# Kernel optimization log

Hardware: AMD Instinct MI355X
Metric: run time of the kernel (lower is better)

Reference implementation:

```python
import jax, jax.numpy as jnp
import numpy as np
import math

H = 512        # hidden_dim
DEPTH = 5
KS = 3         # kernel size
DELTA = 0.1
M = 104        # timestamp == seq_len
NC = 5
B = 512
BN_EPS = 1e-5


def setup_inputs() -> dict:
    key = jax.random.key(0)
    ks = jax.random.split(key, 16)
    inp = {}
    inp['x'] = jax.random.normal(ks[0], (B, 1, M), dtype=jnp.float32)
    # CausalCNN: depth conv layers (first is 1->H, rest H->H), each followed by BN
    inp['conv_w0'] = jax.random.normal(ks[1], (H, 1, KS), dtype=jnp.float32) * (1.0 / np.sqrt(KS))
    inp['conv_b0'] = jnp.zeros((H,), jnp.float32)
    inp['conv_w'] = jax.random.normal(ks[2], (DEPTH - 1, H, H, KS), dtype=jnp.float32) * (1.0 / np.sqrt(H * KS))
    inp['conv_b'] = jnp.zeros((DEPTH - 1, H), jnp.float32)
    inp['bn_gamma'] = jnp.ones((DEPTH, H), jnp.float32)
    inp['bn_beta'] = jnp.zeros((DEPTH, H), jnp.float32)
    # input_proj
    inp['proj_w'] = jax.random.normal(ks[3], (H, H), dtype=jnp.float32) * (1.0 / np.sqrt(H))
    inp['proj_b'] = jnp.zeros((H,), jnp.float32)
    # ZOH layers: A = -0.01*I + 0.001*randn, B = 0.01*randn [H,1], C = 0.01*randn [1,H]
    eye = jnp.eye(H, dtype=jnp.float32)
    inp['A_all'] = -0.01 * eye[None] + 0.001 * jax.random.normal(ks[4], (DEPTH, H, H), dtype=jnp.float32)
    inp['B_all'] = 0.01 * jax.random.normal(ks[5], (DEPTH, H, 1), dtype=jnp.float32)
    inp['C_all'] = 0.01 * jax.random.normal(ks[6], (DEPTH, 1, H), dtype=jnp.float32)
    # fc_temp: Linear(H,H) -> BN1d(H) -> GELU -> Dropout(eval) -> Linear(H,NC)
    inp['fc1_w'] = jax.random.normal(ks[7], (H, H), dtype=jnp.float32) * (1.0 / np.sqrt(H))
    inp['fc1_b'] = jnp.zeros((H,), jnp.float32)
    inp['fc_bn_gamma'] = jnp.ones((H,), jnp.float32)
    inp['fc_bn_beta'] = jnp.zeros((H,), jnp.float32)
    inp['fc2_w'] = jax.random.normal(ks[8], (NC, H), dtype=jnp.float32) * (1.0 / np.sqrt(H))
    inp['fc2_b'] = jnp.zeros((NC,), jnp.float32)
    return inp


def _causal_conv(x, w, b):
    # x: [B, Cin, T], w: [Cout, Cin, K] -> left-pad K-1 (equivalent to pad both + trim right)
    y = jax.lax.conv_general_dilated(x, w, window_strides=(1,), padding=[(KS - 1, 0)],
                                     dimension_numbers=('NCH', 'OIH', 'NCH'))
    return y + b[None, :, None]


def _bn_ct(x, g, b):
    # BatchNorm1d over [B, C, T], batch statistics (training-mode normalization)
    m = x.mean(axis=(0, 2), keepdims=True)
    v = x.var(axis=(0, 2), keepdims=True)
    return g[None, :, None] * (x - m) * jax.lax.rsqrt(v + BN_EPS) + b[None, :, None]


def _pos_encoding(T, d):
    pos = jnp.arange(T, dtype=jnp.float32)[:, None]
    div = jnp.exp(jnp.arange(0, d, 2, dtype=jnp.float32) * (-math.log(10000.0) / d))
    pe = jnp.zeros((T, d), jnp.float32)
    pe = pe.at[:, 0::2].set(jnp.sin(pos * div))
    pe = pe.at[:, 1::2].set(jnp.cos(pos * div))
    return pe


def _zoh_kbar(A, Bv, Cv):
    # A: [H,H], Bv: [H,1], Cv: [1,H] -> normalized K_bar [M]
    A_bar = jax.scipy.linalg.expm(DELTA * A)
    I = jnp.eye(H, dtype=A.dtype)
    A_inv = jnp.linalg.inv(A + 0.001 * I)
    B_bar = A_inv @ (A_bar - I) @ (DELTA * Bv)  # [H,1]
    # term_k = C @ A_bar^k @ B_bar; sequential vector recurrence replaces matrix powers
    def step(v, _):
        term = (Cv @ v)[0, 0]
        return A_bar @ v, term
    _, terms = jax.lax.scan(step, B_bar, None, length=M)  # [M]
    Kb = jnp.flip(terms, axis=0)
    return Kb / (jnp.linalg.norm(Kb) + 1e-6)


def reference(x, conv_w0, conv_b0, conv_w, conv_b, bn_gamma, bn_beta, proj_w, proj_b,
              A_all, B_all, C_all, fc1_w, fc1_b, fc_bn_gamma, fc_bn_beta, fc2_w, fc2_b):
    # CausalCNN
    h = jax.nn.relu(_bn_ct(_causal_conv(x, conv_w0, conv_b0), bn_gamma[0], bn_beta[0]))
    for i in range(DEPTH - 1):
        h = jax.nn.relu(_bn_ct(_causal_conv(h, conv_w[i], conv_b[i]), bn_gamma[i + 1], bn_beta[i + 1]))
    h = jnp.transpose(h, (0, 2, 1))  # [B, T, H]
    # positional encoding + input projection
    h = h + _pos_encoding(M, H)[None]
    h = jnp.einsum('bth,oh->bto', h, proj_w) + proj_b
    # stacked ZOH kernels: each layer multiplies x by its normalized K_bar along time
    Ks = jax.vmap(_zoh_kbar)(A_all, B_all, C_all)  # [DEPTH, M]
    h = h * jnp.prod(Ks, axis=0)[None, :, None]
    # mean pool over time, then fc_temp (BN with batch stats, dropout = identity/eval)
    h = h.mean(axis=1)  # [B, H]
    h = jnp.dot(h, fc1_w.T) + fc1_b
    m = h.mean(axis=0, keepdims=True)
    v = h.var(axis=0, keepdims=True)
    h = fc_bn_gamma * (h - m) * jax.lax.rsqrt(v + BN_EPS) + fc_bn_beta
    h = jax.nn.gelu(h, approximate=False)
    logits = jnp.dot(h, fc2_w.T) + fc2_b  # [B, NC]
    return logits
```

## Files before the change

kernel.cpp:

```cpp
#include <hip/hip_runtime.h>
#include <cstdio>
#include <cmath>
#include <cstdint>

constexpr int BM = 512 * 104;
constexpr float BN_EPS = 1e-5f;

constexpr size_t SZ_BF   = (size_t)BM * 512 * 2;
constexpr size_t SZ_MAT5 = (size_t)5 * 512 * 512 * 4;
constexpr size_t OFF_YB0 = 0;
constexpr size_t OFF_YB1 = OFF_YB0 + SZ_BF;
constexpr size_t OFF_WT2 = OFF_YB1 + SZ_BF;
constexpr size_t OFF_X   = OFF_WT2 + 6291456;
constexpr size_t OFF_T1  = OFF_X   + SZ_MAT5;
constexpr size_t OFF_T2  = OFF_T1  + SZ_MAT5;
constexpr size_t OFF_E   = OFF_T2  + SZ_MAT5;
constexpr size_t OFF_MW  = OFF_E   + SZ_MAT5;
constexpr size_t OFF_P2  = OFF_MW  + SZ_MAT5;
constexpr size_t OFF_P4  = OFF_P2  + SZ_MAT5;
constexpr size_t OFF_ROWT= OFF_P4  + SZ_MAT5;
constexpr size_t OFF_COLS= OFF_ROWT + 655360;
constexpr size_t OFF_COLS2=OFF_COLS + 655360;
constexpr size_t OFF_PIVI= OFF_COLS2 + 655360;
constexpr size_t OFF_PJT = OFF_PIVI + 81920;
// ... 197 lines not shown
        } else if (mode == 5) {
            for (int j = 0; j < 4; ++j) v[j] += aux[col0 + j] * sc2;
        } else if (mode == 7) {
            float pv[4];
            for (int j = 0; j < 4; ++j) {
                int col = col0 + j;
                pv[j] = ((row == col) ? 0.5f : 0.0f) + aux[(long)row * 512 + col] * (1.0f / 6.0f)
                        + v[j] * (1.0f / 24.0f);
            }
            *(float4*)&Cp[base] = make_float4(pv[0], pv[1], pv[2], pv[3]);
        } else if (mode == 8) {
            for (int j = 0; j < 4; ++j) {
                v[j] += aux[col0 + j];
                cs1[j] += v[j]; cs2[j] += v[j] * v[j];
            }
        }
        *(float4*)&C[base] = make_float4(v[0], v[1], v[2], v[3]);
    }
    if (mode == 8) {
        __syncthreads();
        float* s1s = sm;
        float* s2s = sm + 1024;
#pragma unroll
        for (int j = 0; j < 4; ++j) {
            s1s[ty * 64 + tx * 4 + j] = cs1[j];
            s2s[ty * 64 + tx * 4 + j] = cs2[j];
        }
        __syncthreads();
        if (tid < 64) {
            double a = 0.0, b = 0.0;
#pragma unroll
            for (int t = 0; t < 16; ++t) { a += s1s[t * 64 + tid]; b += s2s[t * 64 + tid]; }
            atomicAdd(&st1[n0 + tid], a);
            atomicAdd(&st2[n0 + tid], b);
        }
    }
}

__global__ __launch_bounds__(256) void k_elim3(
    const float* __restrict__ MWin, float* __restrict__ MWout,
    const float* __restrict__ PIVI, float* __restrict__ PIVN,
    const float* __restrict__ COLSc, float* __restrict__ COLSn, int pc, int pcn)
{
    __shared__ float As[64 * 68];
    __shared__ float Rs[64 * 68];
    __shared__ float fv[64];
    __shared__ int perm[64];
    __shared__ int arr[64];
    __shared__ int pividx;
    __shared__ float dv;
    int z = blockIdx.z;
    MWin += (long)z * 262144; MWout += (long)z * 262144;
    PIVI += z * 4096; COLSc += (long)z * 32768; COLSn += (long)z * 32768;
    int m0 = blockIdx.x * 64, n0 = blockIdx.y * 64;
    int tid = threadIdx.x;
    int tx = tid & 15, ty = tid >> 4;

    if (n0 == pc) {
        for (int it = 0; it < 16; ++it) {
            int idx = it * 256 + tid;
            int r = idx >> 6, c = idx & 63;
            Rs[r * 68 + c] = PIVI[r * 64 + c];
        }
        __syncthreads();
    } else {
        {
            int m = tid >> 2, kb = (tid & 3) * 16;
#pragma unroll
            for (int u = 0; u < 4; ++u) {
                float4 v = *(const float4*)&PIVI[m * 64 + kb + u * 4];
                As[(kb + u * 4 + 0) * 68 + m] = v.x;
                As[(kb + u * 4 + 1) * 68 + m] = v.y;
                As[(kb + u * 4 + 2) * 68 + m] = v.z;
                As[(kb + u * 4 + 3) * 68 + m] = v.w;
            }
            int kr = tid >> 2, cb = (tid & 3) * 16;
#pragma unroll
            for (int u = 0; u < 4; ++u)
                *(float4*)&Rs[kr * 68 + cb + u * 4] =
                    *(const float4*)&MWin[(long)(pc + kr) * 512 + n0 + cb + u * 4];
        }
        __syncthreads();
        float acc1[4][4] = {};
#pragma unroll 8
        for (int kk = 0; kk < 64; ++kk) {
            float4 a = *(const float4*)&As[kk * 68 + ty * 4];
            float4 b = *(const float4*)&Rs[kk * 68 + tx * 4];
            float av[4] = {a.x, a.y, a.z, a.w};
            float bv[4] = {b.x, b.y, b.z, b.w};
#pragma unroll
            for (int i = 0; i < 4; ++i)
#pragma unroll
                for (int j = 0; j < 4; ++j)
                    acc1[i][j] = fmaf(av[i], bv[j], acc1[i][j]);
        }
        __syncthreads();
#pragma unroll
        for (int i = 0; i < 4; ++i)
#pragma unroll
            for (int j = 0; j < 4; ++j)
                Rs[(ty * 4 + i) * 68 + tx * 4 + j] = acc1[i][j];
        __syncthreads();
    }

    if (m0 == pc) {
        for (int it = 0; it < 16; ++it) {
            int idx = it * 256 + tid;
            int r = idx >> 6, c = idx & 63;
            float v = Rs[r * 68 + c];
            MWout[(long)(pc + r) * 512 + n0 + c] = v;
            if (n0 == pcn) COLSn[(pc + r) * 64 + c] = v;
        }
        return;
    }
    {
        int m = tid >> 2, kb = (tid & 3) * 16;
#pragma unroll
        for (int u = 0; u < 4; ++u) {
            float4 v = *(const float4*)&COLSc[(m0 + m) * 64 + kb + u * 4];
            As[(kb + u * 4 + 0) * 68 + m] = v.x;
            As[(kb + u * 4 + 1) * 68 + m] = v.y;
            As[(kb + u * 4 + 2) * 68 + m] = v.z;
            As[(kb + u * 4 + 3) * 68 + m] = v.w;
        }
    }
    __syncthreads();
    float acc[4][4] = {};
#pragma unroll 8
    for (int kk = 0; kk < 64; ++kk) {
        float4 a = *(const float4*)&As[kk * 68 + ty * 4];
        float4 b = *(const float4*)&Rs[kk * 68 + tx * 4];
        float av[4] = {a.x, a.y, a.z, a.w};
        float bv[4] = {b.x, b.y, b.z, b.w};
#pragma unroll
        for (int i = 0; i < 4; ++i)
#pragma unroll
            for (int j = 0; j < 4; ++j)
                acc[i][j] = fmaf(av[i], bv[j], acc[i][j]);
    }
    bool inP = (n0 == pc);
    float vsav[4][4];
#pragma unroll
    for (int i = 0; i < 4; ++i) {
        int row = m0 + ty * 4 + i;
        int col0 = n0 + tx * 4;
        long base = (long)row * 512 + col0;
        float ov[4] = {0.f, 0.f, 0.f, 0.f};
        if (!inP) {
            float4 oldv = *(const float4*)&MWin[base];
            ov[0] = oldv.x; ov[1] = oldv.y; ov[2] = oldv.z; ov[3] = oldv.w;
        }
        float v[4];
#pragma unroll
        for (int j = 0; j < 4; ++j) { v[j] = ov[j] - acc[i][j]; vsav[i][j] = v[j]; }
        *(float4*)&MWout[base] = make_float4(v[0], v[1], v[2], v[3]);
        if (n0 == pcn)
            *(float4*)&COLSn[row * 64 + (col0 - pcn)] = make_float4(v[0], v[1], v[2], v[3]);
    }

    if (!(m0 == pcn && n0 == pcn)) return;
    __syncthreads();
    float* mat = As;
#pragma unroll
    for (int i = 0; i < 4; ++i)
#pragma unroll
        for (int j = 0; j < 4; ++j)
            mat[(ty * 4 + i) * 65 + tx * 4 + j] = vsav[i][j];
    __syncthreads();
    for (int j = 0; j < 64; ++j) {
        if (tid < 64) {
            float v = (tid >= j) ? fabsf(mat[tid * 65 + j]) : -1.0f;
            int idx = tid;
#pragma unroll
            for (int off = 32; off; off >>= 1) {
                float ov = __shfl_down(v, off);
                int oi = __shfl_down(idx, off);
                if (ov > v) { v = ov; idx = oi; }
            }
            if (tid == 0) pividx = idx;
        }
        __syncthreads();
        int r = pividx;
        if (tid < 64) {
            if (r != j) {
                float tj = mat[j * 65 + tid], tr = mat[r * 65 + tid];
                mat[j * 65 + tid] = tr; mat[r * 65 + tid] = tj;
            }
            if (tid == 0) perm[j] = r;
        }
        __syncthreads();
        if (tid < 64) {
            float piv = mat[j * 65 + j];
            float d = 1.0f / piv;
            fv[tid] = mat[tid * 65 + j];
            mat[j * 65 + tid] = (tid == j) ? d : mat[j * 65 + tid] * d;
            if (tid == 0) dv = d;
        }
        __syncthreads();
        {
            int i = tid & 63, c0 = (tid >> 6) * 16;
            if (i != j) {
                float f = fv[i];
                float dd = dv;
#pragma unroll
                for (int u = 0; u < 16; ++u) {
                    int c = c0 + u;
                    float val = mat[i * 65 + c] - f * mat[j * 65 + c];
                    if (c == j) val = -f * dd;
                    mat[i * 65 + c] = val;
                }
            }
        }
        __syncthreads();
    }
    if (tid == 0) {
        for (int c = 0; c < 64; ++c) arr[c] = c;
        for (int j = 63; j >= 0; --j) { int r = perm[j]; int t = arr[j]; arr[j] = arr[r]; arr[r] = t; }
    }
    __syncthreads();
    float* Pg = PIVN + z * 4096;
    for (int it = 0; it < 16; ++it) {
        int idx = it * 256 + tid;
        int r = idx >> 6, c = idx & 63;
        Pg[r * 64 + c] = mat[r * 65 + arr[c]];
    }
}

__global__ __launch_bounds__(256) void k_inv64(const float* __restrict__ MW, int pblk, float* __restrict__ PIVI)
{
    __shared__ float mat[64 * 65];
    __shared__ float fv[64];
    __shared__ int perm[64];
    __shared__ int arr[64];
    __shared__ int pividx;
    __shared__ float dv;
    int z = blockIdx.x;
    const float* Mg = MW + (long)z * 262144 + (long)pblk * 64 * 512 + pblk * 64;
    int tid = threadIdx.x;
    for (int it = 0; it < 16; ++it) {
        int idx = it * 256 + tid;
        int r = idx >> 6, c = idx & 63;
        mat[r * 65 + c] = Mg[r * 512 + c];
    }
    __syncthreads();
    for (int j = 0; j < 64; ++j) {
        if (tid < 64) {
            float v = (tid >= j) ? fabsf(mat[tid * 65 + j]) : -1.0f;
            int idx = tid;
#pragma unroll
            for (int off = 32; off; off >>= 1) {
                float ov = __shfl_down(v, off);
                int oi = __shfl_down(idx, off);
                if (ov > v) { v = ov; idx = oi; }
            }
            if (tid == 0) pividx = idx;
        }
        __syncthreads();
        int r = pividx;
        if (tid < 64) {
            if (r != j) {
                float tj = mat[j * 65 + tid], tr = mat[r * 65 + tid];
                mat[j * 65 + tid] = tr; mat[r * 65 + tid] = tj;
            }
            if (tid == 0) perm[j] = r;
        }
        __syncthreads();
        if (tid < 64) {
            float piv = mat[j * 65 + j];
            float d = 1.0f / piv;
            fv[tid] = mat[tid * 65 + j];
            mat[j * 65 + tid] = (tid == j) ? d : mat[j * 65 + tid] * d;
            if (tid == 0) dv = d;
        }
        __syncthreads();
        {
            int i = tid & 63, c0 = (tid >> 6) * 16;
            if (i != j) {
                float f = fv[i];
                float dd = dv;
#pragma unroll
                for (int u = 0; u < 16; ++u) {
                    int c = c0 + u;
                    float val = mat[i * 65 + c] - f * mat[j * 65 + c];
                    if (c == j) val = -f * dd;
                    mat[i * 65 + c] = val;
                }
            }
        }
        __syncthreads();
    }
    if (tid == 0) {
        for (int c = 0; c < 64; ++c) arr[c] = c;
        for (int j = 63; j >= 0; --j) { int r = perm[j]; int t = arr[j]; arr[j] = arr[r]; arr[r] = t; }
    }
    __syncthreads();
    float* Pg = PIVI + z * 4096;
    for (int it = 0; it < 16; ++it) {
        int idx = it * 256 + tid;
        int r = idx >> 6, c = idx & 63;
        Pg[r * 64 + c] = mat[r * 65 + arr[c]];
    }
}

__global__ __launch_bounds__(1024) void k_zoh(const char* __restrict__ ws,
                                              const float* __restrict__ Aall,
                                              const float* __restrict__ Ball)
{
    __shared__ float Vs[8][512];
    __shared__ float Ws[13][512];
    __shared__ float xs[512], us[512], sv[512];
    int z = blockIdx.x;
    const float* E   = (const float*)(ws + OFF_E)  + (long)z * 262144;
    const float* A2p = (const float*)(ws + OFF_X)  + (long)z * 262144;
    const float* A4p = (const float*)(ws + OFF_T1) + (long)z * 262144;
    const float* A8p = (const float*)(ws + OFF_T2) + (long)z * 262144;
    const float* A16p= (const float*)(ws + OFF_P2) + (long)z * 262144;
    const float* A32p= (const float*)(ws + OFF_P4) + (long)z * 262144;
    const float* Mi  = (const float*)(ws + OFF_MW) + (long)z * 262144;
    const float* Aa  = Aall + (long)z * 262144;
    float* Vg = (float*)(ws + OFF_V)  + (long)z * 4096;
    float* Wg = (float*)(ws + OFF_WV) + (long)z * 6656;
    int tid = threadIdx.x, lane = tid & 63, w = tid >> 6;
    if (tid < 512) { xs[tid] = Ball[z * 512 + tid]; Ws[0][tid] = Wg[tid]; }
    __syncthreads();
    for (int r = w * 32; r < w * 32 + 32; ++r) {
        const float* ar = E + (long)r * 512;
        double acc = 0.0;
#pragma unroll
        for (int m = 0; m < 8; ++m) acc += (double)ar[lane + m * 64] * (double)xs[lane + m * 64];
        for (int off = 32; off; off >>= 1) acc += __shfl_down(acc, off);
        if (lane == 0) us[r] = 0.1f * (float)acc;
    }
    __syncthreads();
    for (int r = w * 32; r < w * 32 + 32; ++r) {
        const float* ar = Mi + (long)r * 512;
        double acc = 0.0;
#pragma unroll
        for (int m = 0; m < 8; ++m) acc += (double)ar[lane + m * 64] * (double)us[lane + m * 64];
        for (int off = 32; off; off >>= 1) acc += __shfl_down(acc, off);
        if (lane == 0) Vs[0][r] = 1.0f * (float)acc;
    }
    __syncthreads();
    for (int r = w * 32; r < w * 32 + 32; ++r) {
        const float* ar = Aa + (long)r * 512;
        double acc = 0.0;
#pragma unroll
        for (int m = 0; m < 8; ++m) acc += (double)ar[lane + m * 64] * (double)Vs[0][lane + m * 64];
        for (int off = 32; off; off >>= 1) acc += __shfl_down(acc, off);
        if (lane == 0) {
            float val = 1.0f * (float)acc + 0.001f * Vs[0][r];
            sv[r] = us[r] - val;
        }
    }
    __syncthreads();
    for (int r = w * 32; r < w * 32 + 32; ++r) {
        const float* ar = Mi + (long)r * 512;
        double acc = 0.0;
#pragma unroll
        for (int m = 0; m < 8; ++m) acc += (double)ar[lane + m * 64] * (double)sv[lane + m * 64];
        for (int off = 32; off; off >>= 1) acc += __shfl_down(acc, off);
        if (lane == 0) Vs[0][r] = Vs[0][r] + 1.0f * (float)acc;
    }
    __syncthreads();
    if (w < 8) {
        float xm[8];
#pragma unroll
        for (int m = 0; m < 8; ++m) xm[m] = Vs[0][lane + m * 64];
        for (int r = w * 64; r < w * 64 + 64; ++r) {
            const float* ar = E + (long)r * 512;
            double acc = 0.0;
#pragma unroll
            for (int m = 0; m < 8; ++m) acc += (double)ar[lane + m * 64] * (double)xm[m];
            for (int off = 32; off; off >>= 1) acc += __shfl_down(acc, off);
            if (lane == 0) Vs[1][r] = 1.0f * (float)acc + 1.0f * Vs[0][r];
        }
    } else {
        int c = tid - 512;
        double acc = 0.0;
#pragma unroll 8
        for (int j = 0; j < 512; ++j) acc += (double)A8p[(long)j * 512 + c] * (double)Ws[0][j];
        Ws[1][c] = (float)acc;
    }
    __syncthreads();
    if (w < 8) {
        const float* xv = (w < 4) ? Vs[0] : Vs[1];
        float* yv = (w < 4) ? Vs[2] : Vs[3];
        int r0 = (w & 3) * 128;
        float xm[8];
#pragma unroll
        for (int m = 0; m < 8; ++m) xm[m] = xv[lane + m * 64];
        for (int r = r0; r < r0 + 128; ++r) {
            const float* ar = A2p + (long)r * 512;
            double acc = 0.0;
#pragma unroll
            for (int m = 0; m < 8; ++m) acc += (double)ar[lane + m * 64] * (double)xm[m];
            for (int off = 32; off; off >>= 1) acc += __shfl_down(acc, off);
            if (lane == 0) yv[r] = (float)acc;
        }
    } else {
        const float* xv = (w < 12) ? Ws[0] : Ws[1];
        float* yv = (w < 12) ? Ws[2] : Ws[3];
        int q = (w < 12) ? (tid - 512) : (tid - 768);
        for (int u = 0; u < 2; ++u) {
            int c = q + u * 256;
            double acc = 0.0;
#pragma unroll 8
            for (int j = 0; j < 512; ++j) acc += (double)A16p[(long)j * 512 + c] * (double)xv[j];
            yv[c] = (float)acc;
        }
    }
    __syncthreads();
    if (w < 8) {
        int t = w >> 1, r0 = (w & 1) * 256;
        float xm[8];
#pragma unroll
        for (int m = 0; m < 8; ++m) xm[m] = Vs[t][lane + m * 64];
        for (int r = r0; r < r0 + 256; ++r) {
            const float* ar = A4p + (long)r * 512;
            double acc = 0.0;
#pragma unroll
            for (int m = 0; m < 8; ++m) acc += (double)ar[lane + m * 64] * (double)xm[m];
            for (int off = 32; off; off >>= 1) acc += __shfl_down(acc, off);
            if (lane == 0) Vs[4 + t][r] = (float)acc;
        }
    } else {
        int c = tid - 512;
        double a0 = 0.0, a1 = 0.0, a2 = 0.0, a3 = 0.0;
#pragma unroll 8
        for (int j = 0; j < 512; ++j) {
            double a = (double)A32p[(long)j * 512 + c];
            a0 += a * (double)Ws[0][j]; a1 += a * (double)Ws[1][j];
            a2 += a * (double)Ws[2][j]; a3 += a * (double)Ws[3][j];
        }
        Ws[4][c] = (float)a0; Ws[5][c] = (float)a1; Ws[6][c] = (float)a2; Ws[7][c] = (float)a3;
    }
    __syncthreads();
    if (tid < 512) {
        int c = tid;
        double a0 = 0.0, a1 = 0.0, a2 = 0.0, a3 = 0.0;
#pragma unroll 8
        for (int j = 0; j < 512; ++j) {
            double a = (double)A32p[(long)j * 512 + c];
            a0 += a * (double)Ws[4][j]; a1 += a * (double)Ws[5][j];
            a2 += a * (double)Ws[6][j]; a3 += a * (double)Ws[7][j];
        }
        Ws[8][c] = (float)a0; Ws[9][c] = (float)a1; Ws[10][c] = (float)a2; Ws[11][c] = (float)a3;
    }
    __syncthreads();
    if (tid < 512) {
        double acc = 0.0;
#pragma unroll 8
        for (int j = 0; j < 512; ++j) acc += (double)A32p[(long)j * 512 + tid] * (double)Ws[8][j];
        Ws[12][tid] = (float)acc;
    }
    __syncthreads();
    for (int idx = tid; idx < 8 * 512; idx += 1024) Vg[idx] = ((float*)Vs)[idx];
    for (int idx = tid; idx < 13 * 512; idx += 1024) Wg[idx] = ((float*)Ws)[idx];
}

__global__ __launch_bounds__(256, 2) void k_convm(
    const unsigned short* __restrict__ act,
    const unsigned short* __restrict__ Wt2,
    const float* __restrict__ bias,
    const double* __restrict__ STin,
    const float* __restrict__ gam, const float* __restrict__ bet,
    unsigned short* __restrict__ yout,
    double* __restrict__ s1g, double* __restrict__ s2g,
    const float* __restrict__ WVt, const float* __restrict__ Vt, float* __restrict__ SVECt)
{
    __shared__ __align__(16) unsigned short As[130 * 32];
    __shared__ __align__(16) unsigned short Bs[3 * 256 * 32];
    __shared__ float SCs[512];
    __shared__ float SHs[512];
    __shared__ float invk[5];
    __shared__ float redk[2];
    int tid = threadIdx.x;
    if (blockIdx.x == 416) {
        if (blockIdx.y != 0 || WVt == nullptr) return;
        float* tl = (float*)As;
        for (int t = tid; t < 520; t += 256) {
            int z = t / 104, d = t - z * 104;
            int j = d >> 3, i = d & 7;
            const float* wp = WVt + z * 6656 + j * 512;
            const float* vp = Vt + z * 4096 + i * 512;
            float acc = 0.0f;
#pragma unroll 8
            for (int k = 0; k < 512; ++k) acc += wp[k] * vp[k];
            tl[t] = acc;
        }
        __syncthreads();
        int lane = tid & 63;
        for (int g = tid >> 6; g < 5; g += 4) {
            float a = tl[g * 104 + lane]; a = a * a;
            if (lane < 40) { float b = tl[g * 104 + 64 + lane]; a += b * b; }
#pragma unroll
            for (int off = 32; off; off >>= 1) a += __shfl_down(a, off);
            if (lane == 0) invk[g] = 1.0f / (sqrtf(a) + 1e-6f);
        }
        __syncthreads();
        float s = 0.0f;
        if (tid < 104) {
            s = 1.0f;
            for (int l = 0; l < 5; ++l) s *= tl[l * 104 + (103 - tid)] * invk[l];
            SVECt[tid] = s;
        }
        if (tid < 128) {
            float v = (tid < 104) ? s : 0.0f;
#pragma unroll
            for (int off = 32; off; off >>= 1) v += __shfl_down(v, off);
            if ((tid & 63) == 0) redk[tid >> 6] = v;
        }
        __syncthreads();
        if (tid == 0) SVECt[104] = (redk[0] + redk[1]) * (1.0f / 104.0f);
        return;
    }
    int m0 = blockIdx.x * 128, co0 = blockIdx.y * 256;
    int w = tid >> 6, lane = tid & 63;
    int wr = (w >> 1) * 64, wc = (w & 1) * 128;
    int fr = lane & 15, quad = lane >> 4;

    const double invN = 1.0 / (double)BM;
    for (int c = tid; c < 512; c += 256) {
        double mn = STin[c] * invN;
        double var = STin[512 + c] * invN - mn * mn;
        double rs = 1.0 / sqrt(var + (double)BN_EPS);
        double scd = (double)gam[c] * rs;
        SCs[c] = (float)scd;
        SHs[c] = (float)((double)bet[c] - mn * scd);
    }

    bool valid[4][3];
#pragma unroll
    for (int i = 0; i < 4; ++i) {
        int R = m0 + wr + i * 16 + fr;
        int t = R % 104;
#pragma unroll
        for (int tau = 0; tau < 3; ++tau) valid[i][tau] = (t + tau >= 2);
    }

    int aoff[4][3];
#pragma unroll
    for (int i = 0; i < 4; ++i)
#pragma unroll
        for (int tau = 0; tau < 3; ++tau) {
            int r = wr + i * 16 + fr + tau;
            aoff[i][tau] = r * 32 + (((quad ^ (r >> 1)) & 3) << 3);
        }
    int boff[8];
#pragma unroll
    for (int j = 0; j < 8; ++j) {
        int rb = wc + j * 16 + fr;
        boff[j] = rb * 32 + (((quad ^ (rb >> 1)) & 3) << 3);
    }

    int ka = (tid & 3) * 8;
    int g0 = m0 - 2 + (tid >> 2); if (g0 < 0) g0 = 0;
    int g1 = m0 + 62 + (tid >> 2);
    int g2 = m0 + 126 + (tid >> 2);
    const unsigned short* pa0 = act + (long)g0 * 512 + ka;
    const unsigned short* pa1 = act + (long)g1 * 512 + ka;
    const unsigned short* pa2 = act + (long)g2 * 512 + ka;
    int wbase = (tid >> 2) * 32 + ((((tid & 3) ^ (tid >> 3)) & 3) << 3);
    const unsigned short* pbB = Wt2 + ((long)(co0 + (tid >> 2)) << 9) + ka;

    f32x4 zero4 = {0.f, 0.f, 0.f, 0.f};
    f32x4 acc[4][8];
#pragma unroll
    for (int i = 0; i < 4; ++i)
#pragma unroll
        for (int j = 0; j < 8; ++j) acc[i][j] = zero4;
    bf16x8 zer = {0, 0, 0, 0, 0, 0, 0, 0};

#pragma unroll 1
    for (int s = 0; s < 16; ++s) {
        int ci0 = s * 32;
        __syncthreads();
        uint4 va0 = *(const uint4*)(pa0 + ci0);
        uint4 va1 = *(const uint4*)(pa1 + ci0);
        uint4 va2;
        if (tid < 8) va2 = *(const uint4*)(pa2 + ci0);
#pragma unroll
        for (int tau = 0; tau < 3; ++tau)
#pragma unroll
            for (int it = 0; it < 4; ++it)
                gld16(pbB + tau * 262144 + it * 32768 + ci0, &Bs[(tau * 4 + it) * 2048 + tid * 8]);
        int cb = ci0 + ka;
        float4 s0 = *(const float4*)&SCs[cb], s1v = *(const float4*)&SCs[cb + 4];
        float4 h0 = *(const float4*)&SHs[cb], h1v = *(const float4*)&SHs[cb + 4];
        {
            uint4 pk;
            pk.x = bnrelu_pk(va0.x, s0.x, s0.y, h0.x, h0.y);
            pk.y = bnrelu_pk(va0.y, s0.z, s0.w, h0.z, h0.w);
            pk.z = bnrelu_pk(va0.z, s1v.x, s1v.y, h1v.x, h1v.y);
            pk.w = bnrelu_pk(va0.w, s1v.z, s1v.w, h1v.z, h1v.w);
            *(uint4*)&As[wbase] = pk;
            pk.x = bnrelu_pk(va1.x, s0.x, s0.y, h0.x, h0.y);
            pk.y = bnrelu_pk(va1.y, s0.z, s0.w, h0.z, h0.w);
            pk.z = bnrelu_pk(va1.z, s1v.x, s1v.y, h1v.x, h1v.y);
            pk.w = bnrelu_pk(va1.w, s1v.z, s1v.w, h1v.z, h1v.w);
            *(uint4*)&As[wbase + 2048] = pk;
            if (tid < 8) {
                pk.x = bnrelu_pk(va2.x, s0.x, s0.y, h0.x, h0.y);
                pk.y = bnrelu_pk(va2.y, s0.z, s0.w, h0.z, h0.w);
                pk.z = bnrelu_pk(va2.z, s1v.x, s1v.y, h1v.x, h1v.y);
                pk.w = bnrelu_pk(va2.w, s1v.z, s1v.w, h1v.z, h1v.w);
                *(uint4*)&As[wbase + 4096] = pk;
            }
        }
        __syncthreads();
#pragma unroll
        for (int tau = 0; tau < 3; ++tau) {
            bf16x8 af[4];
#pragma unroll
            for (int i = 0; i < 4; ++i) {
                bf16x8 raw = *(const bf16x8*)&As[aoff[i][tau]];
                af[i] = valid[i][tau] ? raw : zer;
            }
            bf16x8 bfr[8];
#pragma unroll
            for (int j = 0; j < 8; ++j)
                bfr[j] = *(const bf16x8*)&Bs[tau * 8192 + boff[j]];
#pragma unroll
            for (int i = 0; i < 4; ++i)
#pragma unroll
                for (int j = 0; j < 8; ++j)
                    acc[i][j] = __builtin_amdgcn_mfma_f32_16x16x32_bf16(af[i], bfr[j], acc[i][j], 0, 0, 0);
        }
    }
    float bcol[8], s1[8], s2[8];
#pragma unroll
    for (int jt = 0; jt < 8; ++jt) {
        bcol[jt] = bias[co0 + wc + jt * 16 + fr];
        s1[jt] = 0.0f; s2[jt] = 0.0f;
    }
#pragma unroll
    for (int i = 0; i < 4; ++i) {
        int rbase = m0 + wr + i * 16 + quad * 4;
#pragma unroll
        for (int jt = 0; jt < 8; ++jt) {
            int col = co0 + wc + jt * 16 + fr;
#pragma unroll
            for (int r = 0; r < 4; ++r) {
                float v = acc[i][jt][r] + bcol[jt];
                yout[(long)(rbase + r) * 512 + col] = f2bf(v);
                s1[jt] += v; s2[jt] += v * v;
            }
        }
    }
#pragma unroll
    for (int jt = 0; jt < 8; ++jt) {
        s1[jt] += __shfl_xor(s1[jt], 16); s1[jt] += __shfl_xor(s1[jt], 32);
        s2[jt] += __shfl_xor(s2[jt], 16); s2[jt] += __shfl_xor(s2[jt], 32);
    }
    __syncthreads();
    float* st = (float*)As;
    if (lane < 16) {
#pragma unroll
        for (int jt = 0; jt < 8; ++jt) {
            st[w * 128 + jt * 16 + lane] = s1[jt];
            st[512 + w * 128 + jt * 16 + lane] = s2[jt];
        }
    }
    __syncthreads();
    {
        int half = tid >> 7, cl = tid & 127;
        float a = st[half * 128 + cl] + st[(half + 2) * 128 + cl];
        float b = st[512 + half * 128 + cl] + st[512 + (half + 2) * 128 + cl];
        atomicAdd(&s1g[co0 + tid], (double)a);
        atomicAdd(&s2g[co0 + tid], (double)b);
    }
}

__global__ void k_pool(const unsigned short* __restrict__ y4, const double* __restrict__ ST4,
                       const float* __restrict__ gam, const float* __restrict__ bet,
                       const float* __restrict__ svec, float* __restrict__ g)
{
    __shared__ float sl[104];
    int b = blockIdx.x;
    int c = blockIdx.y * 256 + threadIdx.x;
    if (threadIdx.x < 104) sl[threadIdx.x] = svec[threadIdx.x];
    __syncthreads();
    const double invN = 1.0 / (double)BM;
    double mn = ST4[c] * invN;
    double var = ST4[512 + c] * invN - mn * mn;
    double rs = 1.0 / sqrt(var + (double)BN_EPS);
    double scd = (double)gam[c] * rs;
    float sc = (float)scd, sh = (float)((double)bet[c] - mn * scd);
    int he = c & ~1;
    float div = expf((float)he * (-0.017988946039015984f));
    float acc = 0.0f;
    const unsigned short* yb = y4 + (long)b * 104 * 512 + c;
    for (int t = 0; t < 104; ++t) {
        float v = bf2f(yb[t * 512]);
        float hn = fmaxf(fmaf(v, sc, sh), 0.0f);
        float arg = (float)t * div;
        float pe = (c & 1) ? cosf(arg) : sinf(arg);
        acc += sl[t] * (hn + pe);
    }
    g[(long)b * 512 + c] = acc * (1.0f / 104.0f);
}

__global__ __launch_bounds__(256) void k_final(const float* __restrict__ zin, const double* __restrict__ st,
                                               const float* __restrict__ gam, const float* __restrict__ bet,
                                               const float* __restrict__ w2, const float* __restrict__ b2,
                                               float* __restrict__ outp)
{
    __shared__ float red[256];
    int b = blockIdx.x, tid = threadIdx.x;
    int oo[2] = { tid, tid + 256 };
    float gv[2];
#pragma unroll
    for (int q = 0; q < 2; ++q) {
        int o = oo[q];
        double m = st[o] * (1.0 / 512.0);
        double var = st[512 + o] * (1.0 / 512.0) - m * m;
        double rs = 1.0 / sqrt(var + (double)BN_EPS);
        float xn = (float)(((double)zin[(long)b * 512 + o] - m) * rs * (double)gam[o] + (double)bet[o]);
        gv[q] = 0.5f * xn * (1.0f + erff(xn * 0.70710678118654752f));
    }
    for (int n = 0; n < 5; ++n) {
        float p = gv[0] * w2[n * 512 + oo[0]] + gv[1] * w2[n * 512 + oo[1]];
        red[tid] = p;
        __syncthreads();
        for (int off = 128; off; off >>= 1) { if (tid < off) red[tid] += red[tid + off]; __syncthreads(); }
        if (tid == 0) outp[b * 5 + n] = red[0] + b2[n];
        __syncthreads();
    }
}

static void mm(hipStream_t s, int Mt, int Nt, int z,
               const float* A, long sA, int lda,
               const float* B, long sB, int ldb,
               float* C, long sC, int ldc,
               int K, int mode,
               const float* aux = nullptr, long sAux = 0, const float* aux2 = nullptr,
               float* Cp = nullptr, double* st1 = nullptr, double* st2 = nullptr, int pc = 0)
{
    dim3 g(Mt, Nt, z);
    k_mm<<<g, 256, 0, s>>>(A, sA, lda, B, sB, ldb, C, sC, ldc, K, mode, aux, sAux, aux2, Cp, st1, st2, pc);
}

extern "C" void kernel_launch(void* const* d_in, const int* in_sizes, int n_in,
                              void* d_out, int out_size, void* d_ws, size_t ws_size,
                              hipStream_t stream)
{
    (void)in_sizes; (void)n_in; (void)out_size;
    const float* x       = (const float*)d_in[0];
    const float* conv_w0 = (const float*)d_in[1];
    const float* conv_b0 = (const float*)d_in[2];
    const float* conv_w  = (const float*)d_in[3];
    const float* conv_b  = (const float*)d_in[4];
    const float* bn_g    = (const float*)d_in[5];
    const float* bn_b    = (const float*)d_in[6];
    const float* proj_w  = (const float*)d_in[7];
    const float* proj_b  = (const float*)d_in[8];
    const float* A_all   = (const float*)d_in[9];
    const float* B_all   = (const float*)d_in[10];
    const float* C_all   = (const float*)d_in[11];
    const float* fc1_w   = (const float*)d_in[12];
    const float* fc1_b   = (const float*)d_in[13];
    const float* fbn_g   = (const float*)d_in[14];
    const float* fbn_b   = (const float*)d_in[15];
    const float* fc2_w   = (const float*)d_in[16];
    const float* fc2_b   = (const float*)d_in[17];
    float* outp = (float*)d_out;
    char* ws = (char*)d_ws;
    if (ws_size < WS_NEED) { printf("ws too small: %zu < %zu\n", ws_size, WS_NEED); return; }

    unsigned short* YB0 = (unsigned short*)(ws + OFF_YB0);
    unsigned short* YB1 = (unsigned short*)(ws + OFF_YB1);
    unsigned short* WT2 = (unsigned short*)(ws + OFF_WT2);
    float* Xb   = (float*)(ws + OFF_X);
    float* T1   = (float*)(ws + OFF_T1);
    float* T2   = (float*)(ws + OFF_T2);
    float* Eb   = (float*)(ws + OFF_E);
    float* MW   = (float*)(ws + OFF_MW);
    float* P2   = (float*)(ws + OFF_P2);
    float* P4   = (float*)(ws + OFF_P4);
    float* COLS1= (float*)(ws + OFF_COLS);
    float* COLS2= (float*)(ws + OFF_COLS2);
    float* PIVA = (float*)(ws + OFF_PIVI);
    float* PIVB = (float*)(ws + OFF_ROWT);
    float* PJT  = (float*)(ws + OFF_PJT);
    float* F1T  = (float*)(ws + OFF_F1T);
    float* G    = (float*)(ws + OFF_G);
    float* POOL = (float*)(ws + OFF_POOL);
    float* Zb   = (float*)(ws + OFF_Z);
    double* ST  = (double*)(ws + OFF_ST);
    float* V    = (float*)(ws + OFF_V);
    float* WV   = (float*)(ws + OFF_WV);
    float* SVEC = (float*)(ws + OFF_S);

    const long SM = 262144;
    hipMemsetAsync(ws + OFF_ST, 0, 49152, stream);

    k_pre<<<8320, 256, 0, stream>>>(conv_w, WT2, A_all, Xb, MW, COLS1, C_all, WV,
                                    proj_w, PJT, fc1_w, F1T,
                                    x, conv_w0, conv_b0, YB0, ST, ST + 512);

    {
        float* MB[2]  = { MW, P2 };
        float* PB[2]  = { PIVA, PIVB };
        k_inv64<<<5, 256, 0, stream>>>(MW, 0, PB[0]);
        for (int p = 0; p < 8; ++p) {
            int pc = p * 64;
            float* Cc = (p & 1) ? COLS2 : COLS1;
            float* Cn = (p & 1) ? COLS1 : COLS2;
            k_elim3<<<dim3(8, 8, 5), 256, 0, stream>>>(MB[p & 1], MB[(p + 1) & 1],
                                                       PB[p & 1], PB[(p + 1) & 1],
                                                       Cc, Cn, pc, pc + 64);
        }
    }
    mm(stream, 8, 8, 5, Xb, SM, 512, Xb, SM, 512, T2, SM, 512, 512, 7, Xb, SM, nullptr, T1);
    mm(stream, 8, 8, 5, T2, SM, 512, T1, SM, 512, Eb, SM, 512, 512, 2, Xb, SM);
    mm(stream, 8, 8, 5, Eb, SM, 512, Eb, SM, 512, Xb, SM, 512, 512, 1, Eb, SM);
    mm(stream, 8, 8, 5, Xb, SM, 512, Xb, SM, 512, T1, SM, 512, 512, 0);
    mm(stream, 8, 8, 5, T1, SM, 512, T1, SM, 512, T2, SM, 512, 512, 0);
    mm(stream, 8, 8, 5, T2, SM, 512, T2, SM, 512, P2, SM, 512, 512, 0);
    mm(stream, 8, 8, 5, P2, SM, 512, P2, SM, 512, P4, SM, 512, 512, 0);
    k_zoh<<<5, 1024, 0, stream>>>(ws, A_all, B_all);

    for (int l = 1; l <= 4; ++l) {
        unsigned short* inb  = (l & 1) ? YB0 : YB1;
        unsigned short* outb = (l & 1) ? YB1 : YB0;
        dim3 grid(l == 1 ? 417 : 416, 2);
        k_convm<<<grid, 256, 0, stream>>>(inb, WT2 + (size_t)(l - 1) * 3 * 262144,
                                          conv_b + (l - 1) * 512,
                                          ST + (l - 1) * 1024, bn_g + (l - 1) * 512, bn_b + (l - 1) * 512,
                                          outb, ST + l * 1024, ST + l * 1024 + 512,
                                          (l == 1) ? WV : nullptr, V, SVEC);
    }
    k_pool<<<dim3(512, 2), 256, 0, stream>>>(YB0, ST + 4 * 1024, bn_g + 4 * 512, bn_b + 4 * 512, SVEC, G);

    mm(stream, 8, 8, 1, G, 0, 512, PJT, 0, 512, POOL, 0, 512, 512, 5, proj_b, 0, SVEC + 104);
    mm(stream, 8, 8, 1, POOL, 0, 512, F1T, 0, 512, Zb, 0, 512, 512, 8, fc1_b, 0, nullptr, nullptr,
       ST + 5 * 1024, ST + 5 * 1024 + 512);
    k_final<<<512, 256, 0, stream>>>(Zb, ST + 5 * 1024, fbn_g, fbn_b, fc2_w, fc2_b, outp);
}
```

Measured before the change: 1.964 ms.

## Split ZOH matvec chain into wide grids and halve conv output tile width

Replaces the single k_zoh kernel, which ran only 5 blocks of 1024 threads, with a chain of small matvec launches spread across hundreds of blocks, so the ZOH vector computations can use many more compute units. The causal conv kernel tile is narrowed from 256 to 128 output channels with a 4-wide grid, and occupancy is raised to 4 blocks per SIMD group via launch bounds. The trade-off is extra kernel launches, intermediate vectors written through global memory, and less reuse of the A tile per block in the conv. The new code references workspace offsets OFF_U and OFF_SV, which do not appear in the visible code before.

```diff
diff --git a/kernel.cpp b/kernel.cpp
--- a/kernel.cpp
+++ b/kernel.cpp
@@ -523,163 +523,68 @@
     }
 }
 
-__global__ __launch_bounds__(1024) void k_zoh(const char* __restrict__ ws,
-                                              const float* __restrict__ Aall,
-                                              const float* __restrict__ Ball)
+__global__ void k_matvecA(const float* __restrict__ A, long sA,
+                          const float* __restrict__ x, long sx,
+                          float* __restrict__ y, long sy,
+                          const float* __restrict__ sub, long ssub,
+                          float alpha, float beta, int accum)
 {
-    __shared__ float Vs[8][512];
-    __shared__ float Ws[13][512];
-    __shared__ float xs[512], us[512], sv[512];
-    int z = blockIdx.x;
-    const float* E   = (const float*)(ws + OFF_E)  + (long)z * 262144;
-    const float* A2p = (const float*)(ws + OFF_X)  + (long)z * 262144;
-    const float* A4p = (const float*)(ws + OFF_T1) + (long)z * 262144;
-    const float* A8p = (const float*)(ws + OFF_T2) + (long)z * 262144;
-    const float* A16p= (const float*)(ws + OFF_P2) + (long)z * 262144;
-    const float* A32p= (const float*)(ws + OFF_P4) + (long)z * 262144;
-    const float* Mi  = (const float*)(ws + OFF_MW) + (long)z * 262144;
-    const float* Aa  = Aall + (long)z * 262144;
-    float* Vg = (float*)(ws + OFF_V)  + (long)z * 4096;
-    float* Wg = (float*)(ws + OFF_WV) + (long)z * 6656;
-    int tid = threadIdx.x, lane = tid & 63, w = tid >> 6;
-    if (tid < 512) { xs[tid] = Ball[z * 512 + tid]; Ws[0][tid] = Wg[tid]; }
-    __syncthreads();
-    for (int r = w * 32; r < w * 32 + 32; ++r) {
-        const float* ar = E + (long)r * 512;
-        double acc = 0.0;
-#pragma unroll
-        for (int m = 0; m < 8; ++m) acc += (double)ar[lane + m * 64] * (double)xs[lane + m * 64];
-        for (int off = 32; off; off >>= 1) acc += __shfl_down(acc, off);
-        if (lane == 0) us[r] = 0.1f * (float)acc;
-    }
-    __syncthreads();
-    for (int r = w * 32; r < w * 32 + 32; ++r) {
-        const float* ar = Mi + (long)r * 512;
-        double acc = 0.0;
-#pragma unroll
-        for (int m = 0; m < 8; ++m) acc += (double)ar[lane + m * 64] * (double)us[lane + m * 64];
-        for (int off = 32; off; off >>= 1) acc += __shfl_down(acc, off);
-        if (lane == 0) Vs[0][r] = 1.0f * (float)acc;
-    }
-    __syncthreads();
-    for (int r = w * 32; r < w * 32 + 32; ++r) {
-        const float* ar = Aa + (long)r * 512;
-        double acc = 0.0;
-#pragma unroll
-        for (int m = 0; m < 8; ++m) acc += (double)ar[lane + m * 64] * (double)Vs[0][lane + m * 64];
-        for (int off = 32; off; off >>= 1) acc += __shfl_down(acc, off);
-        if (lane == 0) {
-            float val = 1.0f * (float)acc + 0.001f * Vs[0][r];
-            sv[r] = us[r] - val;
-        }
-    }
-    __syncthreads();
-    for (int r = w * 32; r < w * 32 + 32; ++r) {
-        const float* ar = Mi + (long)r * 512;
-        double acc = 0.0;
-#pragma unroll
-        for (int m = 0; m < 8; ++m) acc += (double)ar[lane + m * 64] * (double)sv[lane + m * 64];
-        for (int off = 32; off; off >>= 1) acc += __shfl_down(acc, off);
-        if (lane == 0) Vs[0][r] = Vs[0][r] + 1.0f * (float)acc;
-    }
-    __syncthreads();
-    if (w < 8) {
+    int row = blockIdx.x, z = blockIdx.y, lane = threadIdx.x;
+    A += (long)z * sA; x += (long)z * sx; y += (long)z * sy;
+    if (sub) sub += (long)z * ssub;
+    const float* ar = A + (long)row * 512;
+    double acc = 0.0;
+#pragma unroll
+    for (int m = 0; m < 8; ++m) {
+        int k = lane + m * 64;
+        acc += (double)ar[k] * (double)x[k];
+    }
+    for (int off = 32; off; off >>= 1) acc += __shfl_down(acc, off);
+    if (lane == 0) {
+        float val = alpha * (float)acc + beta * x[row];
+        if (sub) val = sub[row] - val;
+        if (accum) y[row] += val; else y[row] = val;
+    }
+}
+
+struct VWT { long a[8]; long x[8]; long y[8]; float al[8]; float be[8]; int ty[8]; };
+__global__ void k_vw(const char* __restrict__ ws, VWT T)
+{
+    int g = blockIdx.x, z = blockIdx.y, t = blockIdx.z;
+    int lane = threadIdx.x;
+    const float* A = (const float*)(ws + T.a[t]) + (long)z * 262144;
+    int ty = T.ty[t];
+    long vs = ty ? 6656 : 4096;
+    const float* x = (const float*)(ws + T.x[t]) + (long)z * vs;
+    float* yv = (float*)(ws + T.y[t]) + (long)z * vs;
+    if (ty == 0) {
         float xm[8];
 #pragma unroll
-        for (int m = 0; m < 8; ++m) xm[m] = Vs[0][lane + m * 64];
-        for (int r = w * 64; r < w * 64 + 64; ++r) {
-            const float* ar = E + (long)r * 512;
+        for (int m = 0; m < 8; ++m) xm[m] = x[lane + m * 64];
+        float alpha = T.al[t], beta = T.be[t];
+        for (int r0 = 0; r0 < 64; ++r0) {
+            int row = g * 64 + r0;
+            const float* ar = A + (long)row * 512;
             double acc = 0.0;
 #pragma unroll
             for (int m = 0; m < 8; ++m) acc += (double)ar[lane + m * 64] * (double)xm[m];
             for (int off = 32; off; off >>= 1) acc += __shfl_down(acc, off);
-            if (lane == 0) Vs[1][r] = 1.0f * (float)acc + 1.0f * Vs[0][r];
+            if (lane == 0) yv[row] = alpha * (float)acc + beta * x[row];
         }
     } else {
-        int c = tid - 512;
+        __shared__ float xl[512];
+#pragma unroll
+        for (int m = 0; m < 8; ++m) xl[lane + m * 64] = x[lane + m * 64];
+        __syncthreads();
+        int c = g * 64 + lane;
         double acc = 0.0;
 #pragma unroll 8
-        for (int j = 0; j < 512; ++j) acc += (double)A8p[(long)j * 512 + c] * (double)Ws[0][j];
-        Ws[1][c] = (float)acc;
-    }
-    __syncthreads();
-    if (w < 8) {
-        const float* xv = (w < 4) ? Vs[0] : Vs[1];
-        float* yv = (w < 4) ? Vs[2] : Vs[3];
-        int r0 = (w & 3) * 128;
-        float xm[8];
-#pragma unroll
-        for (int m = 0; m < 8; ++m) xm[m] = xv[lane + m * 64];
-        for (int r = r0; r < r0 + 128; ++r) {
-            const float* ar = A2p + (long)r * 512;
-            double acc = 0.0;
-#pragma unroll
-            for (int m = 0; m < 8; ++m) acc += (double)ar[lane + m * 64] * (double)xm[m];
-            for (int off = 32; off; off >>= 1) acc += __shfl_down(acc, off);
-            if (lane == 0) yv[r] = (float)acc;
-        }
-    } else {
-        const float* xv = (w < 12) ? Ws[0] : Ws[1];
-        float* yv = (w < 12) ? Ws[2] : Ws[3];
-        int q = (w < 12) ? (tid - 512) : (tid - 768);
-        for (int u = 0; u < 2; ++u) {
-            int c = q + u * 256;
-            double acc = 0.0;
-#pragma unroll 8
-            for (int j = 0; j < 512; ++j) acc += (double)A16p[(long)j * 512 + c] * (double)xv[j];
-            yv[c] = (float)acc;
-        }
-    }
-    __syncthreads();
-    if (w < 8) {
-        int t = w >> 1, r0 = (w & 1) * 256;
-        float xm[8];
-#pragma unroll
-        for (int m = 0; m < 8; ++m) xm[m] = Vs[t][lane + m * 64];
-        for (int r = r0; r < r0 + 256; ++r) {
-            const float* ar = A4p + (long)r * 512;
-            double acc = 0.0;
-#pragma unroll
-            for (int m = 0; m < 8; ++m) acc += (double)ar[lane + m * 64] * (double)xm[m];
-            for (int off = 32; off; off >>= 1) acc += __shfl_down(acc, off);
-            if (lane == 0) Vs[4 + t][r] = (float)acc;
-        }
-    } else {
-        int c = tid - 512;
-        double a0 = 0.0, a1 = 0.0, a2 = 0.0, a3 = 0.0;
-#pragma unroll 8
-        for (int j = 0; j < 512; ++j) {
-            double a = (double)A32p[(long)j * 512 + c];
-            a0 += a * (double)Ws[0][j]; a1 += a * (double)Ws[1][j];
-            a2 += a * (double)Ws[2][j]; a3 += a * (double)Ws[3][j];
-        }
-        Ws[4][c] = (float)a0; Ws[5][c] = (float)a1; Ws[6][c] = (float)a2; Ws[7][c] = (float)a3;
-    }
-    __syncthreads();
-    if (tid < 512) {
-        int c = tid;
-        double a0 = 0.0, a1 = 0.0, a2 = 0.0, a3 = 0.0;
-#pragma unroll 8
-        for (int j = 0; j < 512; ++j) {
-            double a = (double)A32p[(long)j * 512 + c];
-            a0 += a * (double)Ws[4][j]; a1 += a * (double)Ws[5][j];
-            a2 += a * (double)Ws[6][j]; a3 += a * (double)Ws[7][j];
-        }
-        Ws[8][c] = (float)a0; Ws[9][c] = (float)a1; Ws[10][c] = (float)a2; Ws[11][c] = (float)a3;
-    }
-    __syncthreads();
-    if (tid < 512) {
-        double acc = 0.0;
-#pragma unroll 8
-        for (int j = 0; j < 512; ++j) acc += (double)A32p[(long)j * 512 + tid] * (double)Ws[8][j];
-        Ws[12][tid] = (float)acc;
-    }
-    __syncthreads();
-    for (int idx = tid; idx < 8 * 512; idx += 1024) Vg[idx] = ((float*)Vs)[idx];
-    for (int idx = tid; idx < 13 * 512; idx += 1024) Wg[idx] = ((float*)Ws)[idx];
-}
-
-__global__ __launch_bounds__(256, 2) void k_convm(
+        for (int j = 0; j < 512; ++j) acc += (double)A[(long)j * 512 + c] * (double)xl[j];
+        yv[c] = (float)acc;
+    }
+}
+
+__global__ __launch_bounds__(256, 4) void k_convm(
     const unsigned short* __restrict__ act,
     const unsigned short* __restrict__ Wt2,
     const float* __restrict__ bias,
@@ -690,7 +595,7 @@
     const float* __restrict__ WVt, const float* __restrict__ Vt, float* __restrict__ SVECt)
 {
     __shared__ __align__(16) unsigned short As[130 * 32];
-    __shared__ __align__(16) unsigned short Bs[3 * 256 * 32];
+    __shared__ __align__(16) unsigned short Bs[3 * 128 * 32];
     __shared__ float SCs[512];
     __shared__ float SHs[512];
     __shared__ float invk[5];
@@ -735,9 +640,9 @@
         if (tid == 0) SVECt[104] = (redk[0] + redk[1]) * (1.0f / 104.0f);
         return;
     }
-    int m0 = blockIdx.x * 128, co0 = blockIdx.y * 256;
+    int m0 = blockIdx.x * 128, co0 = blockIdx.y * 128;
     int w = tid >> 6, lane = tid & 63;
-    int wr = (w >> 1) * 64, wc = (w & 1) * 128;
+    int wr = (w >> 1) * 64, wc = (w & 1) * 64;
     int fr = lane & 15, quad = lane >> 4;
 
     const double invN = 1.0 / (double)BM;
@@ -767,9 +672,9 @@
             int r = wr + i * 16 + fr + tau;
             aoff[i][tau] = r * 32 + (((quad ^ (r >> 1)) & 3) << 3);
         }
-    int boff[8];
-#pragma unroll
-    for (int j = 0; j < 8; ++j) {
+    int boff[4];
+#pragma unroll
+    for (int j = 0; j < 4; ++j) {
         int rb = wc + j * 16 + fr;
         boff[j] = rb * 32 + (((quad ^ (rb >> 1)) & 3) << 3);
     }
@@ -785,11 +690,11 @@
     const unsigned short* pbB = Wt2 + ((long)(co0 + (tid >> 2)) << 9) + ka;
 
     f32x4 zero4 = {0.f, 0.f, 0.f, 0.f};
-    f32x4 acc[4][8];
+    f32x4 acc[4][4];
 #pragma unroll
     for (int i = 0; i < 4; ++i)
 #pragma unroll
-        for (int j = 0; j < 8; ++j) acc[i][j] = zero4;
+        for (int j = 0; j < 4; ++j) acc[i][j] = zero4;
     bf16x8 zer = {0, 0, 0, 0, 0, 0, 0, 0};
 
 #pragma unroll 1
@@ -803,8 +708,8 @@
 #pragma unroll
         for (int tau = 0; tau < 3; ++tau)
 #pragma unroll
-            for (int it = 0; it < 4; ++it)
-                gld16(pbB + tau * 262144 + it * 32768 + ci0, &Bs[(tau * 4 + it) * 2048 + tid * 8]);
+            for (int it = 0; it < 2; ++it)
+                gld16(pbB + tau * 262144 + it * 32768 + ci0, &Bs[(tau * 2 + it) * 2048 + tid * 8]);
         int cb = ci0 + ka;
         float4 s0 = *(const float4*)&SCs[cb], s1v = *(const float4*)&SCs[cb + 4];
         float4 h0 = *(const float4*)&SHs[cb], h1v = *(const float4*)&SHs[cb + 4];
@@ -837,28 +742,25 @@
                 bf16x8 raw = *(const bf16x8*)&As[aoff[i][tau]];
                 af[i] = valid[i][tau] ? raw : zer;
             }
-            bf16x8 bfr[8];
-#pragma unroll
-            for (int j = 0; j < 8; ++j)
-                bfr[j] = *(const bf16x8*)&Bs[tau * 8192 + boff[j]];
+            bf16x8 bfr[4];
+#pragma unroll
+            for (int j = 0; j < 4; ++j)
+                bfr[j] = *(const bf16x8*)&Bs[tau * 4096 + boff[j]];
 #pragma unroll
             for (int i = 0; i < 4; ++i)
 #pragma unroll
-                for (int j = 0; j < 8; ++j)
+                for (int j = 0; j < 4; ++j)
                     acc[i][j] = __builtin_amdgcn_mfma_f32_16x16x32_bf16(af[i], bfr[j], acc[i][j], 0, 0, 0);
         }
     }
-    float bcol[8], s1[8], s2[8];
-#pragma unroll
-    for (int jt = 0; jt < 8; ++jt) {
-        bcol[jt] = bias[co0 + wc + jt * 16 + fr];
-        s1[jt] = 0.0f; s2[jt] = 0.0f;
-    }
+    float bcol[4], s1[4] = {0, 0, 0, 0}, s2[4] = {0, 0, 0, 0};
+#pragma unroll
+    for (int jt = 0; jt < 4; ++jt) bcol[jt] = bias[co0 + wc + jt * 16 + fr];
 #pragma unroll
     for (int i = 0; i < 4; ++i) {
         int rbase = m0 + wr + i * 16 + quad * 4;
 #pragma unroll
-        for (int jt = 0; jt < 8; ++jt) {
+        for (int jt = 0; jt < 4; ++jt) {
             int col = co0 + wc + jt * 16 + fr;
 #pragma unroll
             for (int r = 0; r < 4; ++r) {
@@ -869,7 +771,7 @@
         }
     }
 #pragma unroll
-    for (int jt = 0; jt < 8; ++jt) {
+    for (int jt = 0; jt < 4; ++jt) {
         s1[jt] += __shfl_xor(s1[jt], 16); s1[jt] += __shfl_xor(s1[jt], 32);
         s2[jt] += __shfl_xor(s2[jt], 16); s2[jt] += __shfl_xor(s2[jt], 32);
     }
@@ -877,16 +779,16 @@
     float* st = (float*)As;
     if (lane < 16) {
 #pragma unroll
-        for (int jt = 0; jt < 8; ++jt) {
-            st[w * 128 + jt * 16 + lane] = s1[jt];
-            st[512 + w * 128 + jt * 16 + lane] = s2[jt];
+        for (int jt = 0; jt < 4; ++jt) {
+            st[w * 64 + jt * 16 + lane] = s1[jt];
+            st[256 + w * 64 + jt * 16 + lane] = s2[jt];
         }
     }
     __syncthreads();
-    {
-        int half = tid >> 7, cl = tid & 127;
-        float a = st[half * 128 + cl] + st[(half + 2) * 128 + cl];
-        float b = st[512 + half * 128 + cl] + st[512 + (half + 2) * 128 + cl];
+    if (tid < 128) {
+        int w0 = tid >> 6, cl = tid & 63;
+        float a = st[w0 * 64 + cl] + st[(w0 + 2) * 64 + cl];
+        float b = st[256 + w0 * 64 + cl] + st[256 + (w0 + 2) * 64 + cl];
         atomicAdd(&s1g[co0 + tid], (double)a);
         atomicAdd(&s2g[co0 + tid], (double)b);
     }
@@ -1008,6 +910,8 @@
     float* POOL = (float*)(ws + OFF_POOL);
     float* Zb   = (float*)(ws + OFF_Z);
     double* ST  = (double*)(ws + OFF_ST);
+    float* U    = (float*)(ws + OFF_U);
+    float* SV   = (float*)(ws + OFF_SV);
     float* V    = (float*)(ws + OFF_V);
     float* WV   = (float*)(ws + OFF_WV);
     float* SVEC = (float*)(ws + OFF_S);
@@ -1039,12 +943,51 @@
     mm(stream, 8, 8, 5, T1, SM, 512, T1, SM, 512, T2, SM, 512, 512, 0);
     mm(stream, 8, 8, 5, T2, SM, 512, T2, SM, 512, P2, SM, 512, 512, 0);
     mm(stream, 8, 8, 5, P2, SM, 512, P2, SM, 512, P4, SM, 512, 512, 0);
-    k_zoh<<<5, 1024, 0, stream>>>(ws, A_all, B_all);
+    k_matvecA<<<dim3(512, 5), 64, 0, stream>>>(Eb, SM, B_all, 512, U, 512, nullptr, 0, 0.1f, 0.0f, 0);
+    k_matvecA<<<dim3(512, 5), 64, 0, stream>>>(MW, SM, U, 512, V, 4096, nullptr, 0, 1.0f, 0.0f, 0);
+    k_matvecA<<<dim3(512, 5), 64, 0, stream>>>(A_all, SM, V, 4096, SV, 512, U, 512, 1.0f, 0.001f, 0);
+    k_matvecA<<<dim3(512, 5), 64, 0, stream>>>(MW, SM, SV, 512, V, 4096, nullptr, 0, 1.0f, 0.0f, 1);
+    auto Voff = [](int i) { return (long)(OFF_V + (size_t)i * 2048); };
+    auto Woff = [](int j) { return (long)(OFF_WV + (size_t)j * 2048); };
+    {
+        VWT T = {};
+        T.a[0] = OFF_E;  T.x[0] = Voff(0); T.y[0] = Voff(1); T.al[0] = 1; T.be[0] = 1; T.ty[0] = 0;
+        T.a[1] = OFF_T2; T.x[1] = Woff(0); T.y[1] = Woff(1); T.ty[1] = 1;
+        k_vw<<<dim3(8, 5, 2), 64, 0, stream>>>(ws, T);
+    }
+    {
+        VWT T = {};
+        T.a[0] = OFF_X;  T.x[0] = Voff(0); T.y[0] = Voff(2); T.al[0] = 1; T.ty[0] = 0;
+        T.a[1] = OFF_X;  T.x[1] = Voff(1); T.y[1] = Voff(3); T.al[1] = 1; T.ty[1] = 0;
+        T.a[2] = OFF_P2; T.x[2] = Woff(0); T.y[2] = Woff(2); T.ty[2] = 1;
+        T.a[3] = OFF_P2; T.x[3] = Woff(1); T.y[3] = Woff(3); T.ty[3] = 1;
+        k_vw<<<dim3(8, 5, 4), 64, 0, stream>>>(ws, T);
+    }
+    {
+        VWT T = {};
+        for (int i = 0; i < 4; ++i) {
+            T.a[i] = OFF_T1; T.x[i] = Voff(i); T.y[i] = Voff(4 + i); T.al[i] = 1; T.ty[i] = 0;
+            T.a[4 + i] = OFF_P4; T.x[4 + i] = Woff(i); T.y[4 + i] = Woff(4 + i); T.ty[4 + i] = 1;
+        }
+        k_vw<<<dim3(8, 5, 8), 64, 0, stream>>>(ws, T);
+    }
+    {
+        VWT T = {};
+        for (int i = 0; i < 4; ++i) {
+            T.a[i] = OFF_P4; T.x[i] = Woff(4 + i); T.y[i] = Woff(8 + i); T.ty[i] = 1;
+        }
+        k_vw<<<dim3(8, 5, 4), 64, 0, stream>>>(ws, T);
+    }
+    {
+        VWT T = {};
+        T.a[0] = OFF_P4; T.x[0] = Woff(8); T.y[0] = Woff(12); T.ty[0] = 1;
+        k_vw<<<dim3(8, 5, 1), 64, 0, stream>>>(ws, T);
+    }
 
     for (int l = 1; l <= 4; ++l) {
         unsigned short* inb  = (l & 1) ? YB0 : YB1;
         unsigned short* outb = (l & 1) ? YB1 : YB0;
-        dim3 grid(l == 1 ? 417 : 416, 2);
+        dim3 grid(l == 1 ? 417 : 416, 4);
         k_convm<<<grid, 256, 0, stream>>>(inb, WT2 + (size_t)(l - 1) * 3 * 262144,
                                           conv_b + (l - 1) * 512,
                                           ST + (l - 1) * 1024, bn_g + (l - 1) * 512, bn_b + (l - 1) * 512,
```

Result: faster. 1.712 ms (-12.8%).
